# Optimization experiments

Measured on AMD Instinct MI355X. Metric: run time of the kernel, lower is better.

The kernel has to match this reference:

```python
import jax, jax.numpy as jnp
import numpy as np

B, T, D = 64, 4096, 256
CTX = 100

def setup_inputs() -> dict:
    key = jax.random.key(0)
    k1, k2, k3 = jax.random.split(key, 3)
    X = jax.random.normal(k1, (B, T, D), dtype=jnp.float32)
    # keras 'uniform' init is U(-0.05, 0.05); scale matches that regime
    W = jax.random.uniform(k2, (D, CTX), dtype=jnp.float32, minval=-0.05, maxval=0.05)
    u = jax.random.uniform(k3, (CTX, 1), dtype=jnp.float32, minval=-0.05, maxval=0.05)
    return {"X": X, "W": W, "u": u}

def reference(X, W, u):
    # u_tw: (B, T, CTX)
    u_tw = jnp.tanh(jnp.einsum('btd,dc->btc', X, W))
    # tw_stimulus: (B, T) attention logits over timesteps
    logits = jnp.einsum('btc,c->bt', u_tw, u[:, 0])
    att = jax.nn.softmax(logits, axis=-1)           # (B, T)
    # weighted sum over time: (B, D) -- avoids materializing broadcasted weights
    return jnp.einsum('btd,bt->bd', X, att)
```

## Files before the change

kernel.cpp:

```cpp
#include <hip/hip_runtime.h>
#include <hip/hip_bf16.h>


#define NB 64
#define NT_TOK 4096
#define ND 256
#define NCTX 100
#define NTILE 7
#define KSTEPS 8
#define BLOCKS_PER_B 16
#define NBLOCKS (NB * BLOCKS_PER_B)
#define TOK_PER_BLOCK (NT_TOK / BLOCKS_PER_B)
#define TILES_PER_WAVE 4

typedef __attribute__((ext_vector_type(8))) short short8;
typedef __attribute__((ext_vector_type(4))) float f32x4;

#define WS_UPAD_OFF 114688
#define WS_PNUM_OFF 115200
#define WS_PDEN_OFF (115200 + 1048576)

__device__ __forceinline__ unsigned short f2bf(float f) {
  unsigned u = __builtin_bit_cast(unsigned, f);
  u += 0x7FFFu + ((u >> 16) & 1u);
  return (unsigned short)(u >> 16);
}

__device__ __forceinline__ float tanh_fast(float x) {
  float e = __expf(2.0f * x);
  return 1.0f - 2.0f / (e + 1.0f);
}

__global__ void prep_kernel(const float* __restrict__ W, const float* __restrict__ u,
                            unsigned short* __restrict__ wfrag, float* __restrict__ upad) {
  int blk = blockIdx.x;
  int l = threadIdx.x;
  int nt = blk / KSTEPS, s = blk % KSTEPS;
  int col = nt * 16 + (l & 15);
  int kbase = s * 32 + (l >> 4) * 8;
  unsigned short v[8];
#pragma unroll
  for (int j = 0; j < 8; ++j) {
    float f = (col < NCTX) ? W[(size_t)(kbase + j) * NCTX + col] : 0.0f;
    v[j] = f2bf(f);
  }
  unsigned short* dst = wfrag + (size_t)(blk * 64 + l) * 8;
#pragma unroll
  for (int j = 0; j < 8; ++j) dst[j] = v[j];
  if (blk < 2) {
    int c = blk * 64 + l;
    if (c < NTILE * 16) upad[c] = (c < NCTX) ? u[c] : 0.0f;
  }
}

__global__ __launch_bounds__(256, 4) void main_kernel(
    const float* __restrict__ X, const unsigned short* __restrict__ wfrag,
    const float* __restrict__ upad, float* __restrict__ pnum, float* __restrict__ pden) {
  int blk = blockIdx.x;
  int b  = blk / BLOCKS_PER_B;
  int bi = blk % BLOCKS_PER_B;
  int tid = threadIdx.x;
  int wave = tid >> 6;
  int l  = tid & 63;
  int lg = l >> 4;
  int lr = l & 15;
  const float* Xb = X + (size_t)b * NT_TOK * ND;
  int tok_base = bi * TOK_PER_BLOCK + wave * (TILES_PER_WAVE * 16);

  float ucol[NTILE];
#pragma unroll
  for (int nt = 0; nt < NTILE; ++nt) ucol[nt] = upad[nt * 16 + lr];

  float accd[4] = {0.f, 0.f, 0.f, 0.f};
  float accden = 0.f;

  __shared__ float snum[4][ND];
  __shared__ float sden[4];

  for (int tile = 0; tile < TILES_PER_WAVE; ++tile) {
    int tok0 = tok_base + tile * 16;
    f32x4 c[NTILE];
#pragma unroll
    for (int nt = 0; nt < NTILE; ++nt) c[nt] = (f32x4){0.f, 0.f, 0.f, 0.f};

    const float* xrow = Xb + (size_t)(tok0 + lr) * ND + lg * 8;
#pragma unroll 2
    for (int s = 0; s < KSTEPS; ++s) {
      f32x4 a0 = *(const f32x4*)(xrow + s * 32);
      f32x4 a1 = *(const f32x4*)(xrow + s * 32 + 4);
      short8 af;
      af[0] = (short)f2bf(a0[0]); af[1] = (short)f2bf(a0[1]);
      af[2] = (short)f2bf(a0[2]); af[3] = (short)f2bf(a0[3]);
      af[4] = (short)f2bf(a1[0]); af[5] = (short)f2bf(a1[1]);
      af[6] = (short)f2bf(a1[2]); af[7] = (short)f2bf(a1[3]);
#pragma unroll
      for (int nt = 0; nt < NTILE; ++nt) {
        short8 bf = *(const short8*)(wfrag + (size_t)((nt * KSTEPS + s) * 64 + l) * 8);
        c[nt] = __builtin_amdgcn_mfma_f32_16x16x32_bf16(af, bf, c[nt], 0, 0, 0);
      }
    }

    float sj[4];
#pragma unroll
    for (int j = 0; j < 4; ++j) {
      float t = 0.f;
#pragma unroll
      for (int nt = 0; nt < NTILE; ++nt) t = fmaf(tanh_fast(c[nt][j]), ucol[nt], t);
      sj[j] = t;
    }
#pragma unroll
    for (int j = 0; j < 4; ++j) {
      sj[j] += __shfl_xor(sj[j], 1, 64);
      sj[j] += __shfl_xor(sj[j], 2, 64);
      sj[j] += __shfl_xor(sj[j], 4, 64);
      sj[j] += __shfl_xor(sj[j], 8, 64);
    }
    float wj[4];
#pragma unroll
    for (int j = 0; j < 4; ++j) wj[j] = __expf(sj[j]);

#pragma unroll
    for (int t = 0; t < 16; ++t) {
      float wt = __shfl(wj[t & 3], (t >> 2) * 16, 64);
      f32x4 xv = *(const f32x4*)(Xb + (size_t)(tok0 + t) * ND + l * 4);
      accd[0] = fmaf(wt, xv[0], accd[0]);
      accd[1] = fmaf(wt, xv[1], accd[1]);
      accd[2] = fmaf(wt, xv[2], accd[2]);
      accd[3] = fmaf(wt, xv[3], accd[3]);
      accden += wt;
    }
  }

#pragma unroll
  for (int j = 0; j < 4; ++j) snum[wave][l * 4 + j] = accd[j];
  if (l == 0) sden[wave] = accden;
  __syncthreads();
  float s = snum[0][tid] + snum[1][tid] + snum[2][tid] + snum[3][tid];
  pnum[(size_t)blk * ND + tid] = s;
  if (tid == 0) pden[blk] = sden[0] + sden[1] + sden[2] + sden[3];
}

__global__ void fin_kernel(const float* __restrict__ pnum, const float* __restrict__ pden,
                           float* __restrict__ out) {
  int b = blockIdx.x;
  int d = threadIdx.x;
  float num = 0.f, den = 0.f;
#pragma unroll
  for (int i = 0; i < BLOCKS_PER_B; ++i) {
    num += pnum[(size_t)(b * BLOCKS_PER_B + i) * ND + d];
    den += pden[b * BLOCKS_PER_B + i];
  }
  out[b * ND + d] = num / den;
}

extern "C" void kernel_launch(void* const* d_in, const int* in_sizes, int n_in,
                              void* d_out, int out_size, void* d_ws, size_t ws_size,
                              hipStream_t stream) {
  const float* X = (const float*)d_in[0];
  const float* W = (const float*)d_in[1];
  const float* u = (const float*)d_in[2];
  float* out = (float*)d_out;
  char* ws = (char*)d_ws;
  unsigned short* wfrag = (unsigned short*)ws;
  float* upad = (float*)(ws + WS_UPAD_OFF);
  float* pnum = (float*)(ws + WS_PNUM_OFF);
  float* pden = (float*)(ws + WS_PDEN_OFF);

  hipLaunchKernelGGL(prep_kernel, dim3(NTILE * KSTEPS), dim3(64), 0, stream, W, u, wfrag, upad);
  hipLaunchKernelGGL(main_kernel, dim3(NBLOCKS), dim3(256), 0, stream, X, wfrag, upad, pnum, pden);
  hipLaunchKernelGGL(fin_kernel, dim3(NB), dim3(ND), 0, stream, pnum, pden, out);
}
```

Baseline: 396.0 us.

## Software-pipeline X and W fragment loads and double the block count per batch

The MFMA k-loop now prefetches X rows two steps ahead and W fragments one step ahead in register ring buffers, so global load latency overlaps the matrix ops. The weighted-sum phase batches eight X row loads before the FMAs instead of loading one row at a time. Blocks per batch go from 16 to 32 with half the tiles per wave, which raises parallelism but doubles the partial-result traffic. The occupancy hint drops to 3 blocks per SM to leave room for the extra prefetch registers.

```diff
diff --git a/kernel.cpp b/kernel.cpp
--- a/kernel.cpp
+++ b/kernel.cpp
@@ -8,17 +8,17 @@
 #define NCTX 100
 #define NTILE 7
 #define KSTEPS 8
-#define BLOCKS_PER_B 16
+#define BLOCKS_PER_B 32
 #define NBLOCKS (NB * BLOCKS_PER_B)
 #define TOK_PER_BLOCK (NT_TOK / BLOCKS_PER_B)
-#define TILES_PER_WAVE 4
+#define TILES_PER_WAVE 2
 
 typedef __attribute__((ext_vector_type(8))) short short8;
 typedef __attribute__((ext_vector_type(4))) float f32x4;
 
 #define WS_UPAD_OFF 114688
 #define WS_PNUM_OFF 115200
-#define WS_PDEN_OFF (115200 + 1048576)
+#define WS_PDEN_OFF (115200 + 2097152)
 
 __device__ __forceinline__ unsigned short f2bf(float f) {
   unsigned u = __builtin_bit_cast(unsigned, f);
@@ -53,7 +53,7 @@
   }
 }
 
-__global__ __launch_bounds__(256, 4) void main_kernel(
+__global__ __launch_bounds__(256, 3) void main_kernel(
     const float* __restrict__ X, const unsigned short* __restrict__ wfrag,
     const float* __restrict__ upad, float* __restrict__ pnum, float* __restrict__ pden) {
   int blk = blockIdx.x;
@@ -77,6 +77,7 @@
   __shared__ float snum[4][ND];
   __shared__ float sden[4];
 
+#pragma unroll 1
   for (int tile = 0; tile < TILES_PER_WAVE; ++tile) {
     int tok0 = tok_base + tile * 16;
     f32x4 c[NTILE];
@@ -84,20 +85,39 @@
     for (int nt = 0; nt < NTILE; ++nt) c[nt] = (f32x4){0.f, 0.f, 0.f, 0.f};
 
     const float* xrow = Xb + (size_t)(tok0 + lr) * ND + lg * 8;
-#pragma unroll 2
+    const unsigned short* wf_l = wfrag + (size_t)l * 8;
+
+    f32x4 ax[3][2];
+    short8 bfb[2][NTILE];
+    ax[0][0] = *(const f32x4*)(xrow + 0);
+    ax[0][1] = *(const f32x4*)(xrow + 4);
+    ax[1][0] = *(const f32x4*)(xrow + 32);
+    ax[1][1] = *(const f32x4*)(xrow + 36);
+#pragma unroll
+    for (int nt = 0; nt < NTILE; ++nt)
+      bfb[0][nt] = *(const short8*)(wf_l + (size_t)(nt * KSTEPS) * 512);
+
+#pragma unroll
     for (int s = 0; s < KSTEPS; ++s) {
-      f32x4 a0 = *(const f32x4*)(xrow + s * 32);
-      f32x4 a1 = *(const f32x4*)(xrow + s * 32 + 4);
+      const int cur = s % 3;
+      const int far = (s + 2) % 3;
+      const int bcur = s & 1;
+      const int bnxt = (s + 1) & 1;
+      const int s2 = (s + 2 < KSTEPS) ? s + 2 : KSTEPS - 1;
+      ax[far][0] = *(const f32x4*)(xrow + s2 * 32);
+      ax[far][1] = *(const f32x4*)(xrow + s2 * 32 + 4);
+      const int s1 = (s + 1 < KSTEPS) ? s + 1 : KSTEPS - 1;
+#pragma unroll
+      for (int nt = 0; nt < NTILE; ++nt)
+        bfb[bnxt][nt] = *(const short8*)(wf_l + (size_t)(nt * KSTEPS + s1) * 512);
       short8 af;
-      af[0] = (short)f2bf(a0[0]); af[1] = (short)f2bf(a0[1]);
-      af[2] = (short)f2bf(a0[2]); af[3] = (short)f2bf(a0[3]);
-      af[4] = (short)f2bf(a1[0]); af[5] = (short)f2bf(a1[1]);
-      af[6] = (short)f2bf(a1[2]); af[7] = (short)f2bf(a1[3]);
-#pragma unroll
-      for (int nt = 0; nt < NTILE; ++nt) {
-        short8 bf = *(const short8*)(wfrag + (size_t)((nt * KSTEPS + s) * 64 + l) * 8);
-        c[nt] = __builtin_amdgcn_mfma_f32_16x16x32_bf16(af, bf, c[nt], 0, 0, 0);
-      }
+      af[0] = (short)f2bf(ax[cur][0][0]); af[1] = (short)f2bf(ax[cur][0][1]);
+      af[2] = (short)f2bf(ax[cur][0][2]); af[3] = (short)f2bf(ax[cur][0][3]);
+      af[4] = (short)f2bf(ax[cur][1][0]); af[5] = (short)f2bf(ax[cur][1][1]);
+      af[6] = (short)f2bf(ax[cur][1][2]); af[7] = (short)f2bf(ax[cur][1][3]);
+#pragma unroll
+      for (int nt = 0; nt < NTILE; ++nt)
+        c[nt] = __builtin_amdgcn_mfma_f32_16x16x32_bf16(af, bfb[bcur][nt], c[nt], 0, 0, 0);
     }
 
     float sj[4];
@@ -119,15 +139,35 @@
 #pragma unroll
     for (int j = 0; j < 4; ++j) wj[j] = __expf(sj[j]);
 
-#pragma unroll
-    for (int t = 0; t < 16; ++t) {
-      float wt = __shfl(wj[t & 3], (t >> 2) * 16, 64);
-      f32x4 xv = *(const f32x4*)(Xb + (size_t)(tok0 + t) * ND + l * 4);
-      accd[0] = fmaf(wt, xv[0], accd[0]);
-      accd[1] = fmaf(wt, xv[1], accd[1]);
-      accd[2] = fmaf(wt, xv[2], accd[2]);
-      accd[3] = fmaf(wt, xv[3], accd[3]);
-      accden += wt;
+    float wt[16];
+#pragma unroll
+    for (int t = 0; t < 16; ++t)
+      wt[t] = __shfl(wj[t & 3], (t >> 2) * 16, 64);
+#pragma unroll
+    for (int t = 0; t < 16; ++t) accden += wt[t];
+
+    {
+      f32x4 xv[8];
+#pragma unroll
+      for (int j = 0; j < 8; ++j)
+        xv[j] = *(const f32x4*)(Xb + (size_t)(tok0 + j) * ND + l * 4);
+#pragma unroll
+      for (int j = 0; j < 8; ++j) {
+        accd[0] = fmaf(wt[j], xv[j][0], accd[0]);
+        accd[1] = fmaf(wt[j], xv[j][1], accd[1]);
+        accd[2] = fmaf(wt[j], xv[j][2], accd[2]);
+        accd[3] = fmaf(wt[j], xv[j][3], accd[3]);
+      }
+#pragma unroll
+      for (int j = 0; j < 8; ++j)
+        xv[j] = *(const f32x4*)(Xb + (size_t)(tok0 + 8 + j) * ND + l * 4);
+#pragma unroll
+      for (int j = 0; j < 8; ++j) {
+        accd[0] = fmaf(wt[8 + j], xv[j][0], accd[0]);
+        accd[1] = fmaf(wt[8 + j], xv[j][1], accd[1]);
+        accd[2] = fmaf(wt[8 + j], xv[j][2], accd[2]);
+        accd[3] = fmaf(wt[8 + j], xv[j][3], accd[3]);
+      }
     }
   }
 
```

After: 550.5 us. 39.0% more time.
